# Kernel optimization log

Hardware: AMD Instinct MI355X
Metric: run time of the kernel (lower is better)

## Reference

```python
import jax, jax.numpy as jnp
import numpy as np

NUM_HEADS = 16


def setup_inputs() -> dict:
    key = jax.random.key(0)
    k1, k2, k3 = jax.random.split(key, 3)
    B, S, D = 4, 2048, 1024
    x = jax.random.normal(k1, (B, S, D), dtype=jnp.float32)
    w_qkv = jax.random.normal(k2, (D, 3 * D), dtype=jnp.float32) * 0.02
    b_qkv = jnp.zeros((3 * D,), dtype=jnp.float32)
    w_proj = jax.random.normal(k3, (D, D), dtype=jnp.float32) * 0.02
    b_proj = jnp.zeros((D,), dtype=jnp.float32)
    return {"x": x, "w_qkv": w_qkv, "b_qkv": b_qkv, "w_proj": w_proj, "b_proj": b_proj}


def reference(x, w_qkv, b_qkv, w_proj, b_proj):
    B, S, D = x.shape
    H = NUM_HEADS
    hd = D // H
    # fused qkv projection: [B,S,3D] -> [B,S,3H,hd]
    qkv = (x @ w_qkv + b_qkv).reshape(B, S, 3 * H, hd)
    q, k, v = jnp.split(qkv, 3, axis=2)  # each [B,S,H,hd]
    scale = (1.0 / jnp.sqrt(hd)).astype(x.dtype)
    scores = jnp.einsum("bqhd,bkhd->bhqk", q, k) * scale  # [B,H,S,S]
    causal = jnp.tril(jnp.ones((S, S), dtype=bool))  # [S,S]
    masked = jnp.where(causal, scores, jnp.finfo(scores.dtype).min)
    # softmax in fp32 reduce dtype, cast back (dropout_rate=0 -> identity)
    attn = jax.nn.softmax(masked.astype(jnp.float32)).astype(masked.dtype)
    out = jnp.einsum("bhqk,bkhd->bqhd", attn, v).reshape(B, S, D)
    return out @ w_proj + b_proj
```

## Files before the change

kernel.cpp:

```cpp
#include <hip/hip_runtime.h>
#include <hip/hip_bf16.h>

typedef __attribute__((ext_vector_type(8))) short short8;
typedef __attribute__((ext_vector_type(4))) float f32x4;

#define B_   4
#define S_   2048
#define D_   1024
#define H_   16
#define HD_  64
#define M_   (B_ * S_)
#define N3_  (3 * D_)

#define GLDS16(g, l)                                                        \
  __builtin_amdgcn_global_load_lds(                                         \
      (const __attribute__((address_space(1))) void*)(g),                   \
      (__attribute__((address_space(3))) void*)(l), 16, 0, 0)

__device__ __forceinline__ unsigned pack_bf2(float a, float b) {
  union { __hip_bfloat16 h; unsigned short s; } ua, ub;
  ua.h = __float2bfloat16(a);
  ub.h = __float2bfloat16(b);
  return (unsigned)ua.s | ((unsigned)ub.s << 16);
}

__global__ __launch_bounds__(256) void cast_f32_bf16(
    const float* __restrict__ in, __hip_bfloat16* __restrict__ out, int n) {
  int i = (blockIdx.x * 256 + threadIdx.x) * 4;
  if (i + 3 < n) {
    float4 v = *(const float4*)(in + i);
    union { ushort4 u4; __hip_bfloat16 h[4]; } p;
    p.h[0] = __float2bfloat16(v.x);
    p.h[1] = __float2bfloat16(v.y);
    p.h[2] = __float2bfloat16(v.z);
    p.h[3] = __float2bfloat16(v.w);
    *(ushort4*)(out + i) = p.u4;
  }
}

__global__ __launch_bounds__(256) void transpose_cast(
    const float* __restrict__ in, __hip_bfloat16* __restrict__ out,
    int rows, int cols) {
  __shared__ float tile[32][33];
  int bx = blockIdx.x * 32;
  int by = blockIdx.y * 32;
  int tx = threadIdx.x, ty = threadIdx.y;
#pragma unroll
  for (int i = 0; i < 4; ++i)
    tile[ty + i * 8][tx] = in[(size_t)(by + ty + i * 8) * cols + bx + tx];
  __syncthreads();
#pragma unroll
  for (int i = 0; i < 4; ++i)
    out[(size_t)(bx + ty + i * 8) * rows + by + tx] =
        __float2bfloat16(tile[tx][ty + i * 8]);
}

__device__ inline void store_out(float* p, float v) { *p = v; }
__device__ inline void store_out(__hip_bfloat16* p, float v) {
  *p = __float2bfloat16(v);
}

template <typename OUT_T, bool WVT>
__global__ __launch_bounds__(256) void gemm_bt_bias(
    const __hip_bfloat16* __restrict__ A, const __hip_bfloat16* __restrict__ Bt,
    const float* __restrict__ bias, OUT_T* __restrict__ C,
    __hip_bfloat16* __restrict__ vt, int M, int N, int K) {
  __shared__ __align__(16) __hip_bfloat16 Alds[128 * 64];
  __shared__ __align__(16) __hip_bfloat16 Blds[128 * 64];
  const int t = threadIdx.x;
  const int wave = t >> 6, lane = t & 63;
  const int quad = lane >> 4, l15 = lane & 15;
  const int wm = (wave >> 1) * 64, wn = (wave & 1) * 64;
  const int m0 = blockIdx.y * 128, n0 = blockIdx.x * 128;

  const int rsub = lane >> 3;
  const int gc16 = (lane & 7) ^ (rsub & 7);
  const __hip_bfloat16* gA[4];
  const __hip_bfloat16* gB[4];
  __hip_bfloat16* lA[4];
  __hip_bfloat16* lB[4];
#pragma unroll
  for (int i = 0; i < 4; ++i) {
    int c = wave * 4 + i;
    int row = c * 8 + rsub;
    gA[i] = A + (size_t)(m0 + row) * K + gc16 * 8;
    gB[i] = Bt + (size_t)(n0 + row) * K + gc16 * 8;
    lA[i] = Alds + c * 512;
    lB[i] = Blds + c * 512;
  }

  f32x4 acc[4][4] = {};

  for (int k0 = 0; k0 < K; k0 += 64) {
#pragma unroll
    for (int i = 0; i < 4; ++i) {
      GLDS16(gA[i] + k0, lA[i]);
      GLDS16(gB[i] + k0, lB[i]);
    }
    __syncthreads();
#pragma unroll
    for (int kk = 0; kk < 2; ++kk) {
      const int fo = ((kk * 4 + quad) ^ (l15 & 7)) * 8;
      short8 a[4], bfr[4];
#pragma unroll
      for (int mt = 0; mt < 4; ++mt)
        a[mt] = *(const short8*)(Alds + (wm + mt * 16 + l15) * 64 + fo);
#pragma unroll
      for (int nt = 0; nt < 4; ++nt)
        bfr[nt] = *(const short8*)(Blds + (wn + nt * 16 + l15) * 64 + fo);
#pragma unroll
      for (int mt = 0; mt < 4; ++mt)
#pragma unroll
        for (int nt = 0; nt < 4; ++nt)
          acc[mt][nt] = __builtin_amdgcn_mfma_f32_16x16x32_bf16(
              a[mt], bfr[nt], acc[mt][nt], 0, 0, 0);
    }
    __syncthreads();
  }

  if (WVT && n0 >= 2048) {
#pragma unroll
    for (int mt = 0; mt < 4; ++mt)
#pragma unroll
      for (int nt = 0; nt < 4; ++nt) {
        int col = n0 + wn + nt * 16 + l15;
        float bv = bias[col];
        int hv = (col - 2048) >> 6, d = (col - 2048) & 63;
        int row0 = m0 + wm + mt * 16 + quad * 4;
        int bidx = row0 >> 11, s = row0 & 2047;
        uint2 w;
        w.x = pack_bf2(acc[mt][nt][0] + bv, acc[mt][nt][1] + bv);
        w.y = pack_bf2(acc[mt][nt][2] + bv, acc[mt][nt][3] + bv);
        *(uint2*)(vt + ((size_t)(bidx * 16 + hv) * 64 + d) * 2048 + s) = w;
      }
  } else {
#pragma unroll
    for (int mt = 0; mt < 4; ++mt)
#pragma unroll
      for (int nt = 0; nt < 4; ++nt) {
        int col = n0 + wn + nt * 16 + l15;
        float bv = bias[col];
#pragma unroll
        for (int r = 0; r < 4; ++r) {
          int row = m0 + wm + mt * 16 + quad * 4 + r;
          store_out(C + (size_t)row * N + col, acc[mt][nt][r] + bv);
        }
      }
  }
}

__global__ __launch_bounds__(128, 2) void attn_causal(
    const __hip_bfloat16* __restrict__ qkv,
    const __hip_bfloat16* __restrict__ vt,
    __hip_bfloat16* __restrict__ ctx) {
  __shared__ __align__(16) __hip_bfloat16 Klds[2][64 * 64];
  __shared__ __align__(16) __hip_bfloat16 Vlds[2][64 * 64];
  __shared__ __align__(16) __hip_bfloat16 Plds[2][2][16][64];

  const int t = threadIdx.x;
  const int wave = t >> 6, lane = t & 63;
  const int quad = lane >> 4, l15 = lane & 15;

  const int wg = blockIdx.x;
  const int xcd = wg & 7, loc = wg >> 3;
  const int pair = (xcd << 3) | (loc >> 4);
  const int xb = loc & 15;
  const int b = pair >> 4, h = pair & 15;

  const size_t qbase = (size_t)b * S_ * N3_ + h * HD_;
  const size_t kbase = qbase + D_;
  const size_t vtbase = (size_t)(b * H_ + h) * HD_ * S_;
  const float C2 = 0.18033688f;

  short8 ones;
#pragma unroll
  for (int j = 0; j < 8; ++j) ones[j] = (short)0x3F80;

  short8 qf[2][2][2];
#pragma unroll
  for (int sel = 0; sel < 2; ++sel) {
    const int qb = sel ? 31 - xb : xb;
#pragma unroll
    for (int g = 0; g < 2; ++g) {
      const int qrow = qb * 64 + wave * 32 + g * 16 + l15;
      qf[sel][g][0] =
          *(const short8*)(qkv + qbase + (size_t)qrow * N3_ + quad * 8);
      qf[sel][g][1] =
          *(const short8*)(qkv + qbase + (size_t)qrow * N3_ + 32 + quad * 8);
    }
  }

  const int rsub = lane >> 3;
  const int swz = ((lane & 7) ^ rsub) * 8;
  const __hip_bfloat16* gK[4];
  const __hip_bfloat16* gV[4];
  __hip_bfloat16* lK[4];
  __hip_bfloat16* lV[4];
#pragma unroll
  for (int i = 0; i < 4; ++i) {
    const int c = wave * 4 + i;
    gK[i] = qkv + kbase + (size_t)(c * 8 + rsub) * N3_ + swz;
    gV[i] = vt + vtbase + (size_t)(c * 8 + rsub) * S_ + swz;
    lK[i] = &Klds[0][c * 512];
    lV[i] = &Vlds[0][c * 512];
  }

  const int fo0 = (quad ^ (l15 & 7)) * 8;
  const int fo1 = ((4 + quad) ^ (l15 & 7)) * 8;

#pragma unroll
  for (int i = 0; i < 4; ++i) {
    GLDS16(gK[i], lK[i]);
    GLDS16(gV[i], lV[i]);
  }
  __syncthreads();
  int cur = 0;

  for (int sel = 0; sel < 2; ++sel) {
    const int qb = sel ? 31 - xb : xb;

    f32x4 o[2][4] = {};
    float m_r[2] = {-1e30f, -1e30f}, l_r[2] = {0.f, 0.f};

    for (int kb = 0; kb <= qb; ++kb) {
      if (sel == 0 || kb < qb) {
        const size_t nk = (kb < qb) ? (size_t)(kb + 1) : 0;
        const size_t ko = nk * (size_t)(64 * N3_);
        const size_t vo = nk * 64;
        const int nb = (cur ^ 1) * 4096;
#pragma unroll
        for (int i = 0; i < 4; ++i) {
          GLDS16(gK[i] + ko, lK[i] + nb);
          GLDS16(gV[i] + vo, lV[i] + nb);
        }
      }

      const __hip_bfloat16* Kb = &Klds[cur][0];
      const __hip_bfloat16* Vb = &Vlds[cur][0];

      short8 kf[4][2];
#pragma unroll
      for (int nt = 0; nt < 4; ++nt) {
        const __hip_bfloat16* kr = Kb + (nt * 16 + l15) * 64;
        kf[nt][0] = *(const short8*)(kr + fo0);
        kf[nt][1] = *(const short8*)(kr + fo1);
      }

      const bool diag = (kb == qb);
      short8 pB[2][2];
#pragma unroll
      for (int g = 0; g < 2; ++g) {
        f32x4 st[4];
#pragma unroll
        for (int nt = 0; nt < 4; ++nt) {
          f32x4 z = {};
          z = __builtin_amdgcn_mfma_f32_16x16x32_bf16(kf[nt][0], qf[sel][g][0],
                                                      z, 0, 0, 0);
          z = __builtin_amdgcn_mfma_f32_16x16x32_bf16(kf[nt][1], qf[sel][g][1],
                                                      z, 0, 0, 0);
          st[nt] = z;
        }
        if (diag) {
          const int rloc = wave * 32 + g * 16 + l15;
#pragma unroll
          for (int nt = 0; nt < 4; ++nt)
#pragma unroll
            for (int r = 0; r < 4; ++r)
              if (nt * 16 + quad * 4 + r > rloc) st[nt][r] = -1e30f;
        }

        float tm = st[0][0];
#pragma unroll
        for (int nt = 0; nt < 4; ++nt)
#pragma unroll
          for (int r = 0; r < 4; ++r) tm = fmaxf(tm, st[nt][r]);
        tm = fmaxf(tm, __shfl_xor(tm, 16));
        tm = fmaxf(tm, __shfl_xor(tm, 32));
        const float pm = tm * C2;

        if (!__all(pm - m_r[g] <= 8.0f)) {
          const float mn = fmaxf(m_r[g], pm);
          const float al = __builtin_amdgcn_exp2f(m_r[g] - mn);
          m_r[g] = mn;
          l_r[g] *= al;
#pragma unroll
          for (int dt = 0; dt < 4; ++dt)
#pragma unroll
            for (int r = 0; r < 4; ++r) o[g][dt][r] *= al;
        }
        const float mneg = -m_r[g];

        __hip_bfloat16* prow = &Plds[wave][g][l15][0];
#pragma unroll
        for (int nt = 0; nt < 4; ++nt) {
          float p0 =
              __builtin_amdgcn_exp2f(__builtin_fmaf(st[nt][0], C2, mneg));
          float p1 =
              __builtin_amdgcn_exp2f(__builtin_fmaf(st[nt][1], C2, mneg));
          float p2 =
              __builtin_amdgcn_exp2f(__builtin_fmaf(st[nt][2], C2, mneg));
          float p3 =
              __builtin_amdgcn_exp2f(__builtin_fmaf(st[nt][3], C2, mneg));
          uint2 w;
          w.x = pack_bf2(p0, p1);
          w.y = pack_bf2(p2, p3);
          const int u = nt * 2 + (quad >> 1);
          *(uint2*)(prow + ((u ^ (l15 & 7)) * 8 + (quad & 1) * 4)) = w;
        }
        pB[g][0] = *(const short8*)(prow + fo0);
        pB[g][1] = *(const short8*)(prow + fo1);

        f32x4 ps = {};
        ps = __builtin_amdgcn_mfma_f32_16x16x32_bf16(ones, pB[g][0], ps,
                                                     0, 0, 0);
        ps = __builtin_amdgcn_mfma_f32_16x16x32_bf16(ones, pB[g][1], ps,
                                                     0, 0, 0);
        l_r[g] += ps[0];
      }

      short8 vf[4][2];
#pragma unroll
      for (int dt = 0; dt < 4; ++dt) {
        const __hip_bfloat16* vr = Vb + (dt * 16 + l15) * 64;
        vf[dt][0] = *(const short8*)(vr + fo0);
        vf[dt][1] = *(const short8*)(vr + fo1);
      }
#pragma unroll
      for (int dt = 0; dt < 4; ++dt)
#pragma unroll
        for (int g = 0; g < 2; ++g) {
          o[g][dt] = __builtin_amdgcn_mfma_f32_16x16x32_bf16(
              vf[dt][0], pB[g][0], o[g][dt], 0, 0, 0);
          o[g][dt] = __builtin_amdgcn_mfma_f32_16x16x32_bf16(
              vf[dt][1], pB[g][1], o[g][dt], 0, 0, 0);
        }

      __syncthreads();
      cur ^= 1;
    }

#pragma unroll
    for (int g = 0; g < 2; ++g) {
      const float rl = __builtin_amdgcn_rcpf(l_r[g]);
      const int qrow = qb * 64 + wave * 32 + g * 16 + l15;
      __hip_bfloat16* crow = ctx + ((size_t)b * S_ + qrow) * D_ + h * HD_;
#pragma unroll
      for (int dt = 0; dt < 4; ++dt) {
        uint2 w;
        w.x = pack_bf2(o[g][dt][0] * rl, o[g][dt][1] * rl);
        w.y = pack_bf2(o[g][dt][2] * rl, o[g][dt][3] * rl);
        *(uint2*)(crow + dt * 16 + quad * 4) = w;
      }
    }
  }
}

extern "C" void kernel_launch(void* const* d_in, const int* in_sizes, int n_in,
                              void* d_out, int out_size, void* d_ws,
                              size_t ws_size, hipStream_t stream) {
  const float* x      = (const float*)d_in[0];
  const float* w_qkv  = (const float*)d_in[1];
  const float* b_qkv  = (const float*)d_in[2];
  const float* w_proj = (const float*)d_in[3];
  const float* b_proj = (const float*)d_in[4];
  float* out = (float*)d_out;

  char* ws = (char*)d_ws;
  __hip_bfloat16* xb     = (__hip_bfloat16*)(ws + 0);
  __hip_bfloat16* wqkvT  = (__hip_bfloat16*)(ws + 16777216);
  __hip_bfloat16* wprojT = (__hip_bfloat16*)(ws + 23068672);
  __hip_bfloat16* qkvb   = (__hip_bfloat16*)(ws + 25165824);
  __hip_bfloat16* ctx    = (__hip_bfloat16*)(ws + 75497472);
  __hip_bfloat16* vt2    = (__hip_bfloat16*)(ws + 91750400);

  cast_f32_bf16<<<8192, 256, 0, stream>>>(x, xb, M_ * D_);
  transpose_cast<<<dim3(N3_ / 32, D_ / 32), dim3(32, 8), 0, stream>>>(
      w_qkv, wqkvT, D_, N3_);
  transpose_cast<<<dim3(D_ / 32, D_ / 32), dim3(32, 8), 0, stream>>>(
      w_proj, wprojT, D_, D_);

  gemm_bt_bias<__hip_bfloat16, true>
      <<<dim3(N3_ / 128, M_ / 128), 256, 0, stream>>>(
          xb, wqkvT, b_qkv, qkvb, vt2, M_, N3_, D_);

  attn_causal<<<1024, 128, 0, stream>>>(qkvb, vt2, ctx);

  gemm_bt_bias<float, false><<<dim3(D_ / 128, M_ / 128), 256, 0, stream>>>(
      ctx, wprojT, b_proj, out, (__hip_bfloat16*)nullptr, M_, D_, D_);
}
```

Measured before the change: 280.8 us.

## Switch attention to 32x32x16 MFMA and build P fragments in registers

Rewrites the attention inner loop to use 32x32x16 bf16 MFMA tiles instead of 16x16x32, so each wave holds one 32-row query tile with 16-element accumulators. The softmax probabilities are converted to B-operand fragments in registers with cross-half lane shuffles, removing the P round trip through LDS. Q fragments are now loaded per sel pass instead of all up front. This cuts LDS traffic and MFMA issue count, but uses more accumulator registers and adds shuffle instructions.

```diff
diff --git a/kernel.cpp b/kernel.cpp
--- a/kernel.cpp
+++ b/kernel.cpp
@@ -3,6 +3,7 @@
 
 typedef __attribute__((ext_vector_type(8))) short short8;
 typedef __attribute__((ext_vector_type(4))) float f32x4;
+typedef __attribute__((ext_vector_type(16))) float f32x16;
 
 #define B_   4
 #define S_   2048
@@ -155,11 +156,11 @@
     __hip_bfloat16* __restrict__ ctx) {
   __shared__ __align__(16) __hip_bfloat16 Klds[2][64 * 64];
   __shared__ __align__(16) __hip_bfloat16 Vlds[2][64 * 64];
-  __shared__ __align__(16) __hip_bfloat16 Plds[2][2][16][64];
 
   const int t = threadIdx.x;
   const int wave = t >> 6, lane = t & 63;
-  const int quad = lane >> 4, l15 = lane & 15;
+  const int r31 = lane & 31, a5 = lane >> 5;
+  const int xr = r31 & 7;
 
   const int wg = blockIdx.x;
   const int xcd = wg & 7, loc = wg >> 3;
@@ -175,20 +176,6 @@
   short8 ones;
 #pragma unroll
   for (int j = 0; j < 8; ++j) ones[j] = (short)0x3F80;
-
-  short8 qf[2][2][2];
-#pragma unroll
-  for (int sel = 0; sel < 2; ++sel) {
-    const int qb = sel ? 31 - xb : xb;
-#pragma unroll
-    for (int g = 0; g < 2; ++g) {
-      const int qrow = qb * 64 + wave * 32 + g * 16 + l15;
-      qf[sel][g][0] =
-          *(const short8*)(qkv + qbase + (size_t)qrow * N3_ + quad * 8);
-      qf[sel][g][1] =
-          *(const short8*)(qkv + qbase + (size_t)qrow * N3_ + 32 + quad * 8);
-    }
-  }
 
   const int rsub = lane >> 3;
   const int swz = ((lane & 7) ^ rsub) * 8;
@@ -205,9 +192,6 @@
     lV[i] = &Vlds[0][c * 512];
   }
 
-  const int fo0 = (quad ^ (l15 & 7)) * 8;
-  const int fo1 = ((4 + quad) ^ (l15 & 7)) * 8;
-
 #pragma unroll
   for (int i = 0; i < 4; ++i) {
     GLDS16(gK[i], lK[i]);
@@ -216,11 +200,35 @@
   __syncthreads();
   int cur = 0;
 
+#define MKFRAG(sv, Bofs, OUT)                                          \
+  {                                                                    \
+    unsigned dA0 = pack_bf2(sv[Bofs + 0], sv[Bofs + 1]);               \
+    unsigned dA1 = pack_bf2(sv[Bofs + 2], sv[Bofs + 3]);               \
+    unsigned dB0 = pack_bf2(sv[Bofs + 4], sv[Bofs + 5]);               \
+    unsigned dB1 = pack_bf2(sv[Bofs + 6], sv[Bofs + 7]);               \
+    unsigned c0 = (unsigned)__shfl_xor((int)(a5 ? dA0 : dB0), 32);     \
+    unsigned c1 = (unsigned)__shfl_xor((int)(a5 ? dA1 : dB1), 32);     \
+    union { unsigned u[4]; short8 s8; } pu;                            \
+    pu.u[0] = a5 ? c0 : dA0;                                           \
+    pu.u[1] = a5 ? c1 : dA1;                                           \
+    pu.u[2] = a5 ? dB0 : c0;                                           \
+    pu.u[3] = a5 ? dB1 : c1;                                           \
+    OUT = pu.s8;                                                       \
+  }
+
   for (int sel = 0; sel < 2; ++sel) {
     const int qb = sel ? 31 - xb : xb;
-
-    f32x4 o[2][4] = {};
-    float m_r[2] = {-1e30f, -1e30f}, l_r[2] = {0.f, 0.f};
+    const int qrow = qb * 64 + wave * 32 + r31;
+    const int rlq = wave * 32 + r31;
+
+    short8 qf[4];
+#pragma unroll
+    for (int dc = 0; dc < 4; ++dc)
+      qf[dc] = *(const short8*)(qkv + qbase + (size_t)qrow * N3_ +
+                                dc * 16 + a5 * 8);
+
+    f32x16 o0 = {}, o1 = {};
+    float m_r = -1e30f, l_r = 0.f;
 
     for (int kb = 0; kb <= qb; ++kb) {
       if (sel == 0 || kb < qb) {
@@ -238,121 +246,96 @@
       const __hip_bfloat16* Kb = &Klds[cur][0];
       const __hip_bfloat16* Vb = &Vlds[cur][0];
 
-      short8 kf[4][2];
-#pragma unroll
-      for (int nt = 0; nt < 4; ++nt) {
-        const __hip_bfloat16* kr = Kb + (nt * 16 + l15) * 64;
-        kf[nt][0] = *(const short8*)(kr + fo0);
-        kf[nt][1] = *(const short8*)(kr + fo1);
-      }
-
-      const bool diag = (kb == qb);
-      short8 pB[2][2];
-#pragma unroll
-      for (int g = 0; g < 2; ++g) {
-        f32x4 st[4];
-#pragma unroll
-        for (int nt = 0; nt < 4; ++nt) {
-          f32x4 z = {};
-          z = __builtin_amdgcn_mfma_f32_16x16x32_bf16(kf[nt][0], qf[sel][g][0],
-                                                      z, 0, 0, 0);
-          z = __builtin_amdgcn_mfma_f32_16x16x32_bf16(kf[nt][1], qf[sel][g][1],
-                                                      z, 0, 0, 0);
-          st[nt] = z;
+      short8 kf0[4], kf1[4];
+#pragma unroll
+      for (int dc = 0; dc < 4; ++dc) {
+        const int u = ((dc * 2 + a5) ^ xr) * 8;
+        kf0[dc] = *(const short8*)(Kb + r31 * 64 + u);
+        kf1[dc] = *(const short8*)(Kb + (32 + r31) * 64 + u);
+      }
+
+      f32x16 s0 = {}, s1 = {};
+#pragma unroll
+      for (int dc = 0; dc < 4; ++dc) {
+        s0 = __builtin_amdgcn_mfma_f32_32x32x16_bf16(kf0[dc], qf[dc], s0,
+                                                     0, 0, 0);
+        s1 = __builtin_amdgcn_mfma_f32_32x32x16_bf16(kf1[dc], qf[dc], s1,
+                                                     0, 0, 0);
+      }
+
+      if (kb == qb) {
+#pragma unroll
+        for (int reg = 0; reg < 16; ++reg) {
+          const int kl = (reg & 3) + 8 * (reg >> 2) + 4 * a5;
+          if (kl > rlq) s0[reg] = -1e30f;
+          if (kl + 32 > rlq) s1[reg] = -1e30f;
         }
-        if (diag) {
-          const int rloc = wave * 32 + g * 16 + l15;
-#pragma unroll
-          for (int nt = 0; nt < 4; ++nt)
-#pragma unroll
-            for (int r = 0; r < 4; ++r)
-              if (nt * 16 + quad * 4 + r > rloc) st[nt][r] = -1e30f;
-        }
-
-        float tm = st[0][0];
-#pragma unroll
-        for (int nt = 0; nt < 4; ++nt)
-#pragma unroll
-          for (int r = 0; r < 4; ++r) tm = fmaxf(tm, st[nt][r]);
-        tm = fmaxf(tm, __shfl_xor(tm, 16));
-        tm = fmaxf(tm, __shfl_xor(tm, 32));
-        const float pm = tm * C2;
-
-        if (!__all(pm - m_r[g] <= 8.0f)) {
-          const float mn = fmaxf(m_r[g], pm);
-          const float al = __builtin_amdgcn_exp2f(m_r[g] - mn);
-          m_r[g] = mn;
-          l_r[g] *= al;
-#pragma unroll
-          for (int dt = 0; dt < 4; ++dt)
-#pragma unroll
-            for (int r = 0; r < 4; ++r) o[g][dt][r] *= al;
-        }
-        const float mneg = -m_r[g];
-
-        __hip_bfloat16* prow = &Plds[wave][g][l15][0];
-#pragma unroll
-        for (int nt = 0; nt < 4; ++nt) {
-          float p0 =
-              __builtin_amdgcn_exp2f(__builtin_fmaf(st[nt][0], C2, mneg));
-          float p1 =
-              __builtin_amdgcn_exp2f(__builtin_fmaf(st[nt][1], C2, mneg));
-          float p2 =
-              __builtin_amdgcn_exp2f(__builtin_fmaf(st[nt][2], C2, mneg));
-          float p3 =
-              __builtin_amdgcn_exp2f(__builtin_fmaf(st[nt][3], C2, mneg));
-          uint2 w;
-          w.x = pack_bf2(p0, p1);
-          w.y = pack_bf2(p2, p3);
-          const int u = nt * 2 + (quad >> 1);
-          *(uint2*)(prow + ((u ^ (l15 & 7)) * 8 + (quad & 1) * 4)) = w;
-        }
-        pB[g][0] = *(const short8*)(prow + fo0);
-        pB[g][1] = *(const short8*)(prow + fo1);
-
-        f32x4 ps = {};
-        ps = __builtin_amdgcn_mfma_f32_16x16x32_bf16(ones, pB[g][0], ps,
+      }
+
+      float tm = s0[0];
+#pragma unroll
+      for (int reg = 1; reg < 16; ++reg) tm = fmaxf(tm, s0[reg]);
+#pragma unroll
+      for (int reg = 0; reg < 16; ++reg) tm = fmaxf(tm, s1[reg]);
+      tm = fmaxf(tm, __shfl_xor(tm, 32));
+      const float pm = tm * C2;
+
+      if (!__all(pm - m_r <= 8.0f)) {
+        const float mn = fmaxf(m_r, pm);
+        const float al = __builtin_amdgcn_exp2f(m_r - mn);
+        m_r = mn;
+        l_r *= al;
+        o0 *= al;
+        o1 *= al;
+      }
+      const float mneg = -m_r;
+
+#pragma unroll
+      for (int reg = 0; reg < 16; ++reg) {
+        s0[reg] = __builtin_amdgcn_exp2f(__builtin_fmaf(s0[reg], C2, mneg));
+        s1[reg] = __builtin_amdgcn_exp2f(__builtin_fmaf(s1[reg], C2, mneg));
+      }
+
+      short8 pf[4];
+      MKFRAG(s0, 0, pf[0]);
+      MKFRAG(s0, 8, pf[1]);
+      MKFRAG(s1, 0, pf[2]);
+      MKFRAG(s1, 8, pf[3]);
+
+      f32x16 ps = {};
+#pragma unroll
+      for (int kc = 0; kc < 4; ++kc)
+        ps = __builtin_amdgcn_mfma_f32_32x32x16_bf16(ones, pf[kc], ps,
                                                      0, 0, 0);
-        ps = __builtin_amdgcn_mfma_f32_16x16x32_bf16(ones, pB[g][1], ps,
-                                                     0, 0, 0);
-        l_r[g] += ps[0];
-      }
-
-      short8 vf[4][2];
-#pragma unroll
-      for (int dt = 0; dt < 4; ++dt) {
-        const __hip_bfloat16* vr = Vb + (dt * 16 + l15) * 64;
-        vf[dt][0] = *(const short8*)(vr + fo0);
-        vf[dt][1] = *(const short8*)(vr + fo1);
-      }
-#pragma unroll
-      for (int dt = 0; dt < 4; ++dt)
-#pragma unroll
-        for (int g = 0; g < 2; ++g) {
-          o[g][dt] = __builtin_amdgcn_mfma_f32_16x16x32_bf16(
-              vf[dt][0], pB[g][0], o[g][dt], 0, 0, 0);
-          o[g][dt] = __builtin_amdgcn_mfma_f32_16x16x32_bf16(
-              vf[dt][1], pB[g][1], o[g][dt], 0, 0, 0);
-        }
+      l_r += ps[0];
+
+#pragma unroll
+      for (int kc = 0; kc < 4; ++kc) {
+        const int u = ((kc * 2 + a5) ^ xr) * 8;
+        short8 v0 = *(const short8*)(Vb + r31 * 64 + u);
+        short8 v1 = *(const short8*)(Vb + (32 + r31) * 64 + u);
+        o0 = __builtin_amdgcn_mfma_f32_32x32x16_bf16(v0, pf[kc], o0, 0, 0, 0);
+        o1 = __builtin_amdgcn_mfma_f32_32x32x16_bf16(v1, pf[kc], o1, 0, 0, 0);
+      }
 
       __syncthreads();
       cur ^= 1;
     }
 
-#pragma unroll
-    for (int g = 0; g < 2; ++g) {
-      const float rl = __builtin_amdgcn_rcpf(l_r[g]);
-      const int qrow = qb * 64 + wave * 32 + g * 16 + l15;
-      __hip_bfloat16* crow = ctx + ((size_t)b * S_ + qrow) * D_ + h * HD_;
-#pragma unroll
-      for (int dt = 0; dt < 4; ++dt) {
-        uint2 w;
-        w.x = pack_bf2(o[g][dt][0] * rl, o[g][dt][1] * rl);
-        w.y = pack_bf2(o[g][dt][2] * rl, o[g][dt][3] * rl);
-        *(uint2*)(crow + dt * 16 + quad * 4) = w;
-      }
+    const float rl = __builtin_amdgcn_rcpf(l_r);
+    __hip_bfloat16* crow = ctx + ((size_t)b * S_ + qrow) * D_ + h * HD_;
+#pragma unroll
+    for (int q2 = 0; q2 < 4; ++q2) {
+      uint2 w;
+      w.x = pack_bf2(o0[q2 * 4 + 0] * rl, o0[q2 * 4 + 1] * rl);
+      w.y = pack_bf2(o0[q2 * 4 + 2] * rl, o0[q2 * 4 + 3] * rl);
+      *(uint2*)(crow + 8 * q2 + 4 * a5) = w;
+      w.x = pack_bf2(o1[q2 * 4 + 0] * rl, o1[q2 * 4 + 1] * rl);
+      w.y = pack_bf2(o1[q2 * 4 + 2] * rl, o1[q2 * 4 + 3] * rl);
+      *(uint2*)(crow + 32 + 8 * q2 + 4 * a5) = w;
     }
   }
+#undef MKFRAG
 }
 
 extern "C" void kernel_launch(void* const* d_in, const int* in_sizes, int n_in,
```

Measured after the change: 274.2 us. 1.02x faster.
